# Performance work log

Hardware: AMD Instinct MI355X
Metric: run time of the kernel (lower is better)

The kernel has to match this reference:

```python
import jax, jax.numpy as jnp
import numpy as np

ALPHA = 0.1       # args.alpha
T = 1.0           # args.T temperature
SIGMA = 64.0      # Gaussian kernel bandwidth of kernel_function
B_CONST = 1.0     # B in get_lambda
N_ITERS = 50      # 2^-50 << tol=1e-8, matches the break condition of the 1000-iter loop
HW = 256          # image resolution (upsample target)


def _features(feat):
    # get_feature: bilinear upsample (align_corners=False == half-pixel, as jax.image.resize) then sigmoid(x/T)
    n, c, _, _ = feat.shape
    up = jax.image.resize(feat, (n, c, HW, HW), method='bilinear')
    return jax.nn.sigmoid(up / T)


def setup_inputs() -> dict:
    key = jax.random.key(0)
    k1, k2, k3, k4 = jax.random.split(key, 4)
    return {
        'cal_feat': jax.random.normal(k1, (256, 1, 64, 64), jnp.float32),
        'test_feat': jax.random.normal(k2, (32, 1, 64, 64), jnp.float32),
        'cal_gt': jax.random.randint(k3, (256, 1, 256, 256), 0, 2, jnp.int32),
        'test_gt': jax.random.randint(k4, (32, 1, 256, 256), 0, 2, jnp.int32),
    }


def reference(cal_feat, test_feat, cal_gt, test_gt):
    cal_res = _features(cal_feat)    # [N,1,H,W] in (0,1)
    test_res = _features(test_feat)  # [B,1,H,W]
    N = cal_res.shape[0]
    B = test_res.shape[0]
    f32 = cal_res.dtype

    # kernel_function.get_weight: Gaussian RBF on flattened features, plus self-weight 1, row-normalized -> [B, N+1]
    cf = cal_res.reshape(N, -1)
    tf = test_res.reshape(B, -1)
    d2 = (tf * tf).sum(-1)[:, None] + (cf * cf).sum(-1)[None, :] - 2.0 * (tf @ cf.T)
    k = jnp.exp(-d2 / (2.0 * SIGMA * SIGMA))
    w = jnp.concatenate([k, jnp.ones((B, 1), f32)], axis=1)
    w = w / w.sum(axis=1, keepdims=True)

    # FNR_i(t) = #{positive pixels of cal sample i with score < t} / #positives
    # (pred = res >= t, so false negatives are positive pixels with res < t). Precompute sorted
    # positive-pixel scores per cal sample so the bisection is a batched searchsorted.
    gt = (cal_gt > 0).reshape(N, -1)
    pos = jnp.sum(gt, axis=1)                                    # [N]
    scores = jnp.where(gt, cal_res.reshape(N, -1), jnp.inf)
    sorted_scores = jnp.sort(scores, axis=1)                     # [N, HW*HW], padding at +inf
    pos_f = jnp.maximum(pos, 1).astype(f32)

    def fnr_at(t):  # t: [B] thresholds -> [N, B]
        cnt = jax.vmap(lambda s: jnp.searchsorted(s, t, side='left'))(sorted_scores)
        return cnt.astype(f32) / pos_f[:, None]

    # batched bisection on lambda (get_lambda, vectorized over the B test samples)
    def body(carry, _):
        low, high = carry
        lam = 0.5 * (low + high)
        fnr = fnr_at(1.0 - lam)                                   # [N, B]
        risk = jnp.einsum('bn,nb->b', w[:, :-1], fnr) + w[:, -1] * B_CONST
        high = jnp.where(risk < ALPHA, lam, high)
        low = jnp.where(risk >= ALPHA, lam, low)
        return (low, high), None

    init = (jnp.zeros((B,), f32), jnp.ones((B,), f32))
    (low, _), _ = jax.lax.scan(body, init, None, length=N_ITERS)
    lam = low  # _lambda = low after the loop

    # prediction set, size and per-test FNR (get_fnr_list on the test sample)
    pred = test_res >= (1.0 - lam)[:, None, None, None]           # [B,1,H,W] bool
    size = jnp.sum(pred, axis=(1, 2, 3)).astype(f32)
    tgt = test_gt > 0
    tp = jnp.sum(pred & tgt, axis=(1, 2, 3)).astype(f32)
    tpos = jnp.maximum(jnp.sum(tgt, axis=(1, 2, 3)), 1).astype(f32)
    fnr_test = 1.0 - tp / tpos                                    # fdr_tensor, [B]
    return fnr_test, lam, size
```

## Files before the change

kernel.cpp:

```cpp
#include <hip/hip_runtime.h>


#define NPIX 65536
#define HB 16256
#define CDF_STRIDE 16272
#define ALPHA 0.1f

#define OFF_TESTRES  0
#define OFF_CALBF    8388608u
#define OFF_TESTBF   41943040u
#define OFF_GROUPED  46137344u
#define OFF_CDF      79691776u
#define OFF_GPART    96354304u
#define OFF_CC       98451456u
#define OFF_TT       98452480u
#define OFF_THR      98452608u
#define OFF_LAM      98452736u
#define OFF_FACC     98452864u

typedef __attribute__((ext_vector_type(8))) short bf16x8;
typedef __attribute__((ext_vector_type(16))) float f32x16;

__device__ __forceinline__ unsigned short f2bf_rne(float f) {
  unsigned u = __float_as_uint(f);
  return (unsigned short)((u + 0x7FFFu + ((u >> 16) & 1u)) >> 16);
}

__device__ __forceinline__ float score_at(const float* __restrict__ sfeat,
                                          int x0, int x1, float wx, int y) {
  float sy = 0.25f * (float)y - 0.375f;
  int y0 = (int)floorf(sy);
  float wy = sy - (float)y0;
  int y1 = y0 + 1;
  if (y0 < 0) y0 = 0;
  if (y1 > 63) y1 = 63;
  float a = sfeat[y0 * 64 + x0] * (1.f - wx) + sfeat[y0 * 64 + x1] * wx;
  float b = sfeat[y1 * 64 + x0] * (1.f - wx) + sfeat[y1 * 64 + x1] * wx;
  float v = a * (1.f - wy) + b * wy;
  return 1.f / (1.f + __expf(-v));
}

__global__ __launch_bounds__(1024, 8) void k_calt(const float* __restrict__ featc,
                                                  const int* __restrict__ gt,
                                                  unsigned short* __restrict__ calbf,
                                                  unsigned* __restrict__ cdf,
                                                  unsigned short* __restrict__ grouped,
                                                  float* __restrict__ cc,
                                                  const float* __restrict__ featt,
                                                  float* __restrict__ tres,
                                                  unsigned short* __restrict__ tbf,
                                                  float* __restrict__ tt) {
  __shared__ unsigned smem[16384];
  __shared__ float sfeat[4096];
  const int tid = threadIdx.x;
  const int lane = tid & 63, wv = tid >> 6;
  const int x = tid & 255, yq = tid >> 8;
  float sx = 0.25f * (float)x - 0.375f;
  int x0 = (int)floorf(sx);
  float wx = sx - (float)x0;
  int x1 = x0 + 1;
  if (x0 < 0) x0 = 0;
  if (x1 > 63) x1 = 63;

  if (blockIdx.x >= 256) {
    const int b = blockIdx.x - 256;
    for (int i = tid; i < 4096; i += 1024) sfeat[i] = featt[b * 4096 + i];
    __syncthreads();
    float* resb = tres + (size_t)b * NPIX;
    unsigned short* tbn = tbf + (size_t)b * NPIX;
    float sumsq = 0.f;
    #pragma unroll 4
    for (int it = 0; it < 64; ++it) {
      int y = it * 4 + yq;
      float s = score_at(sfeat, x0, x1, wx, y);
      int p = (y << 8) + x;
      resb[p] = s;
      unsigned short bh = f2bf_rne(s);
      tbn[p] = bh;
      float sr = __uint_as_float((unsigned)bh << 16);
      sumsq += sr * sr;
    }
    #pragma unroll
    for (int off = 32; off; off >>= 1) sumsq += __shfl_xor(sumsq, off);
    if (lane == 0) smem[wv] = __float_as_uint(sumsq);
    __syncthreads();
    if (tid == 0) {
      float t = 0.f;
      for (int w = 0; w < 16; ++w) t += __uint_as_float(smem[w]);
      tt[b] = t;
    }
    return;
  }

  const int n = blockIdx.x;
  for (int i = tid; i < HB; i += 1024) smem[i] = 0;
  for (int i = tid; i < 4096; i += 1024) sfeat[i] = featc[n * 4096 + i];
  const int* gtn = gt + (size_t)n * NPIX;
  unsigned short* cbn = calbf + (size_t)n * NPIX;
  __syncthreads();
  unsigned long long pm = 0ull;
  float sumsq = 0.f;
  #pragma unroll 4
  for (int it = 0; it < 64; ++it) {
    int y = it * 4 + yq;
    float s = score_at(sfeat, x0, x1, wx, y);
    int p = (y << 8) + x;
    unsigned short bh = f2bf_rne(s);
    cbn[p] = bh;
    float sr = __uint_as_float((unsigned)bh << 16);
    sumsq += sr * sr;
    if (gtn[p] > 0) {
      pm |= (1ull << it);
      atomicAdd(&smem[__float_as_uint(s) >> 16], 1u);
    }
  }
  #pragma unroll
  for (int off = 32; off; off >>= 1) sumsq += __shfl_xor(sumsq, off);
  if (lane == 0) smem[16336 + wv] = __float_as_uint(sumsq);
  __syncthreads();
  if (tid == 0) {
    float c = 0.f;
    for (int w = 0; w < 16; ++w) c += __uint_as_float(smem[16336 + w]);
    cc[n] = c;
  }
  unsigned* cdfn = cdf + (size_t)n * CDF_STRIDE;
  if (tid < 256) {
    const int base = tid * 64;
    unsigned psum = 0;
    if (base < HB) {
      for (int j = 0; j < 64; ++j) psum += smem[base + ((j + tid) & 63)];
    }
    unsigned inc = psum;
    #pragma unroll
    for (int off = 1; off < 64; off <<= 1) {
      unsigned v = __shfl_up(inc, off);
      if (lane >= off) inc += v;
    }
    if (lane == 63) smem[16320 + wv] = inc;
  }
  __syncthreads();
  if (tid < 256) {
    const int base = tid * 64;
    unsigned psum = 0;
    if (base < HB) {
      for (int j = 0; j < 64; ++j) psum += smem[base + ((j + tid) & 63)];
    }
    unsigned inc = psum;
    #pragma unroll
    for (int off = 1; off < 64; off <<= 1) {
      unsigned v = __shfl_up(inc, off);
      if (lane >= off) inc += v;
    }
    unsigned woff = 0;
    for (int w = 0; w < wv; ++w) woff += smem[16320 + w];
    unsigned run = woff + inc - psum;
    if (base < HB) {
      for (int j = 0; j < 64; ++j) {
        unsigned hcnt = smem[base + j];
        cdfn[base + j] = run;
        smem[base + j] = run;
        run += hcnt;
      }
    }
    if (tid == 255) cdfn[HB] = woff + inc;
  }
  __syncthreads();
  unsigned short* gn = grouped + (size_t)n * NPIX;
  for (int it = 0; it < 64; ++it) {
    if (pm & (1ull << it)) {
      int y = it * 4 + yq;
      float s = score_at(sfeat, x0, x1, wx, y);
      unsigned bits = __float_as_uint(s);
      unsigned idx = atomicAdd(&smem[bits >> 16], 1u);
      gn[idx] = (unsigned short)(bits & 0xFFFFu);
    }
  }
}

__global__ __launch_bounds__(256) void k_gemm(const unsigned short* __restrict__ tbf,
                                              const unsigned short* __restrict__ cbf,
                                              float* __restrict__ gpart) {
  __shared__ __align__(16) unsigned short As[16384];
  __shared__ __align__(16) unsigned short Bs[16384];
  __shared__ float lred[4][1024];
  const int tid = threadIdx.x;
  const int lane = tid & 63, wv = tid >> 6;
  const int r = lane & 31, half = lane >> 5;
  const int nt = blockIdx.x;
  f32x16 acc;
  #pragma unroll
  for (int i = 0; i < 16; ++i) acc[i] = 0.f;
  for (int ch = 0; ch < 2; ++ch) {
    const size_t kbase = (size_t)blockIdx.y * 1024 + ch * 512;
    __syncthreads();
    #pragma unroll
    for (int s = 0; s < 16; ++s) {
      int flat = s * 256 + tid;
      int rem = flat & 2047;
      int row = rem >> 6, kb = rem & 63;
      const unsigned short* src = (flat >= 2048)
          ? cbf + (size_t)(nt * 32 + row) * NPIX + kbase + kb * 8
          : tbf + (size_t)row * NPIX + kbase + kb * 8;
      int slot = ((kb << 5) + row) ^ (kb & 31);
      int4 v = *(const int4*)src;
      *(int4*)((flat >= 2048 ? Bs : As) + slot * 8) = v;
    }
    __syncthreads();
    #pragma unroll
    for (int i = 0; i < 8; ++i) {
      int k8 = (wv << 4) + i * 2 + half;
      int slot = ((k8 << 5) + r) ^ (k8 & 31);
      bf16x8 a = *(const bf16x8*)(As + slot * 8);
      bf16x8 b = *(const bf16x8*)(Bs + slot * 8);
      acc = __builtin_amdgcn_mfma_f32_32x32x16_bf16(a, b, acc, 0, 0, 0);
    }
  }
  #pragma unroll
  for (int rg = 0; rg < 16; ++rg) {
    int m = (rg & 3) + 8 * (rg >> 2) + 4 * half;
    lred[wv][m * 32 + r] = acc[rg];
  }
  __syncthreads();
  float* gp = gpart + (size_t)(blockIdx.y * 8 + nt) * 1024;
  for (int e = tid; e < 1024; e += 256)
    gp[e] = lred[0][e] + lred[1][e] + lred[2][e] + lred[3][e];
}

__global__ __launch_bounds__(512) void k_quant(const float* __restrict__ gpart,
                                               const float* __restrict__ cc,
                                               const float* __restrict__ tt,
                                               const unsigned* __restrict__ cdf,
                                               const unsigned short* __restrict__ grouped,
                                               float* __restrict__ lam,
                                               float* __restrict__ thr,
                                               int* __restrict__ facc) {
  __shared__ float qs[256];
  __shared__ float bins[4096];
  __shared__ float red[8];
  __shared__ float bc[2];
  __shared__ unsigned sBin;
  const int b = blockIdx.x, tid = threadIdx.x;
  const int lane = tid & 63, wv = tid >> 6;

  if (tid < 4) facc[b * 4 + tid] = 0;
  for (int i = tid; i < 4096; i += 512) bins[i] = 0.f;
  if (tid == 0) sBin = 0xFFFFFFFFu;

  float k = 0.f;
  if (tid < 256) {
    const float* gp = gpart + ((tid >> 5) * 1024) + (b * 32) + (tid & 31);
    float g = 0.f;
    #pragma unroll 8
    for (int ks = 0; ks < 64; ++ks) g += gp[(size_t)ks * 8192];
    float d2 = tt[b] + cc[tid] - 2.f * g;
    k = expf(-d2 * (1.f / 8192.f));
  }
  float v = k;
  #pragma unroll
  for (int off = 32; off; off >>= 1) v += __shfl_xor(v, off);
  if (lane == 0) red[wv] = v;
  __syncthreads();
  if (tid == 0) {
    float ws = 1.f;
    for (int w = 0; w < 8; ++w) ws += red[w];
    bc[0] = ws;
  }
  __syncthreads();
  const float wsum = bc[0];
  const float wlast = 1.f / wsum;
  const float R = ALPHA - wlast;
  if (R <= 0.f) {
    if (tid == 0) { lam[b] = 1.0f; thr[b] = 0.0f; }
    return;
  }
  if (tid < 256) {
    unsigned pos = cdf[(size_t)tid * CDF_STRIDE + HB];
    qs[tid] = k / (wsum * (float)(pos ? pos : 1u));
  }
  __syncthreads();

  int lo = 0, hi = HB;
  float baseS = 0.f;
  for (int it = 0; it < 14; ++it) {
    int mid = (lo + hi) >> 1;
    float p = 0.f;
    if (tid < 256) p = qs[tid] * (float)cdf[(size_t)tid * CDF_STRIDE + mid];
    float r = p;
    #pragma unroll
    for (int off = 32; off; off >>= 1) r += __shfl_xor(r, off);
    if (lane == 0) red[wv] = r;
    __syncthreads();
    if (tid == 0) {
      float s = 0.f;
      for (int w = 0; w < 8; ++w) s += red[w];
      bc[1] = s;
    }
    __syncthreads();
    float S = bc[1];
    if (S < R) { lo = mid; baseS = S; } else { hi = mid; }
  }
  const int B = lo;

  {
    const int n = tid >> 1;
    const float q = qs[n];
    const unsigned* cn = cdf + (size_t)n * CDF_STRIDE;
    const unsigned short* gn = grouped + (size_t)n * NPIX;
    unsigned e0 = cn[B + 1];
    for (unsigned j = cn[B] + (tid & 1); j < e0; j += 2)
      atomicAdd(&bins[gn[j] >> 4], q);
  }
  __syncthreads();

  if (wv == 0) {
    float s = 0.f;
    for (int j = 0; j < 64; ++j) s += bins[lane * 64 + j];
    float inc = s;
    #pragma unroll
    for (int off = 1; off < 64; off <<= 1) {
      float u = __shfl_up(inc, off);
      if (lane >= off) inc += u;
    }
    float pre = inc - s;
    bool hit = (baseS + pre < R) && (baseS + inc >= R);
    unsigned long long m = __ballot(hit);
    int ow = m ? (__ffsll((unsigned long long)m) - 1) : -1;
    if (lane == ow) {
      float run = baseS + pre;
      unsigned bin = (unsigned)lane * 64 + 63;
      for (int j = 0; j < 64; ++j) {
        float bv = bins[lane * 64 + j];
        if (run + bv >= R) { bin = (unsigned)lane * 64 + j; break; }
        run += bv;
      }
      sBin = bin;
    }
    if (m == 0 && lane == 0) sBin = 4095u;
  }
  __syncthreads();
  if (tid == 0) {
    unsigned tb = ((unsigned)B << 16) | (sBin << 4);
    lam[b] = 1.0f - __uint_as_float(tb | 0x8u);
    thr[b] = __uint_as_float((tb | 0xFu) + 1u);
  }
}

__global__ __launch_bounds__(256) void k_finalp(const float* __restrict__ tres,
                                                const int* __restrict__ tgt,
                                                const float* __restrict__ thr,
                                                int* __restrict__ facc) {
  __shared__ int red[12];
  const int b = blockIdx.x, seg = blockIdx.y, tid = threadIdx.x;
  const int lane = tid & 63, wv = tid >> 6;
  const float th = thr[b];
  const float* rb = tres + (size_t)b * NPIX + seg * 8192;
  const int* gb = tgt + (size_t)b * NPIX + seg * 8192;
  int sz = 0, tp = 0, tpos = 0;
  for (int i = 0; i < 32; ++i) {
    int p = i * 256 + tid;
    int pred = (rb[p] >= th) ? 1 : 0;
    int tg = (gb[p] > 0) ? 1 : 0;
    sz += pred;
    tp += pred & tg;
    tpos += tg;
  }
  #pragma unroll
  for (int off = 32; off; off >>= 1) {
    sz += __shfl_xor(sz, off);
    tp += __shfl_xor(tp, off);
    tpos += __shfl_xor(tpos, off);
  }
  if (lane == 0) { red[wv] = sz; red[4 + wv] = tp; red[8 + wv] = tpos; }
  __syncthreads();
  if (tid == 0) {
    int s0 = red[0] + red[1] + red[2] + red[3];
    int s1 = red[4] + red[5] + red[6] + red[7];
    int s2 = red[8] + red[9] + red[10] + red[11];
    atomicAdd(&facc[b * 4 + 0], s0);
    atomicAdd(&facc[b * 4 + 1], s1);
    atomicAdd(&facc[b * 4 + 2], s2);
  }
}

__global__ void k_out(const int* __restrict__ facc, const float* __restrict__ lam,
                      float* __restrict__ out) {
  int b = threadIdx.x;
  if (b < 32) {
    int sz = facc[b * 4], tp = facc[b * 4 + 1], tpos = facc[b * 4 + 2];
    float tposf = (float)(tpos > 0 ? tpos : 1);
    out[b] = 1.f - (float)tp / tposf;
    out[32 + b] = lam[b];
    out[64 + b] = (float)sz;
  }
}

extern "C" void kernel_launch(void* const* d_in, const int* in_sizes, int n_in,
                              void* d_out, int out_size, void* d_ws, size_t ws_size,
                              hipStream_t stream) {
  const float* cal_feat = (const float*)d_in[0];
  const float* test_feat = (const float*)d_in[1];
  const int* cal_gt = (const int*)d_in[2];
  const int* test_gt = (const int*)d_in[3];
  float* out = (float*)d_out;
  char* ws = (char*)d_ws;

  float* test_res = (float*)(ws + OFF_TESTRES);
  unsigned short* cal_bf = (unsigned short*)(ws + OFF_CALBF);
  unsigned short* test_bf = (unsigned short*)(ws + OFF_TESTBF);
  unsigned short* grouped = (unsigned short*)(ws + OFF_GROUPED);
  unsigned* cdf = (unsigned*)(ws + OFF_CDF);
  float* gpart = (float*)(ws + OFF_GPART);
  float* cc = (float*)(ws + OFF_CC);
  float* tt = (float*)(ws + OFF_TT);
  float* thr = (float*)(ws + OFF_THR);
  float* lam = (float*)(ws + OFF_LAM);
  int* facc = (int*)(ws + OFF_FACC);

  k_calt<<<dim3(288), dim3(1024), 0, stream>>>(cal_feat, cal_gt, cal_bf, cdf, grouped, cc,
                                               test_feat, test_res, test_bf, tt);
  k_gemm<<<dim3(8, 64), dim3(256), 0, stream>>>(test_bf, cal_bf, gpart);
  k_quant<<<dim3(32), dim3(512), 0, stream>>>(gpart, cc, tt, cdf, grouped, lam, thr, facc);
  k_finalp<<<dim3(32, 8), dim3(256), 0, stream>>>(test_res, test_gt, thr, facc);
  k_out<<<dim3(1), dim3(64), 0, stream>>>(facc, lam, out);
}
```

Before: 245.7 us.

## Fold test feature upsampling into calibration blocks and move test norms to quant kernel

Removes the 32 separate test-sample blocks from the first kernel. Each of the 256 calibration blocks now upsamples 32 rows of one test image after its own work, reading the test features directly from global memory. The test squared-norm reduction moves into k_quant, which re-reads the bf16 test image. The CDF is now written to global in one coalesced pass from shared memory instead of inside the serial per-thread scan loop. Unroll and occupancy hints are also changed. The aim is to balance the tail of the first kernel and to cut strided global writes, at the cost of extra work serialized in k_quant.

```diff
diff --git a/kernel.cpp b/kernel.cpp
--- a/kernel.cpp
+++ b/kernel.cpp
@@ -13,10 +13,9 @@
 #define OFF_CDF      79691776u
 #define OFF_GPART    96354304u
 #define OFF_CC       98451456u
-#define OFF_TT       98452480u
-#define OFF_THR      98452608u
-#define OFF_LAM      98452736u
-#define OFF_FACC     98452864u
+#define OFF_THR      98452480u
+#define OFF_LAM      98452608u
+#define OFF_FACC     98452736u
 
 typedef __attribute__((ext_vector_type(8))) short bf16x8;
 typedef __attribute__((ext_vector_type(16))) float f32x16;
@@ -26,7 +25,7 @@
   return (unsigned short)((u + 0x7FFFu + ((u >> 16) & 1u)) >> 16);
 }
 
-__device__ __forceinline__ float score_at(const float* __restrict__ sfeat,
+__device__ __forceinline__ float score_at(const float* __restrict__ src,
                                           int x0, int x1, float wx, int y) {
   float sy = 0.25f * (float)y - 0.375f;
   int y0 = (int)floorf(sy);
@@ -34,73 +33,40 @@
   int y1 = y0 + 1;
   if (y0 < 0) y0 = 0;
   if (y1 > 63) y1 = 63;
-  float a = sfeat[y0 * 64 + x0] * (1.f - wx) + sfeat[y0 * 64 + x1] * wx;
-  float b = sfeat[y1 * 64 + x0] * (1.f - wx) + sfeat[y1 * 64 + x1] * wx;
+  float a = src[y0 * 64 + x0] * (1.f - wx) + src[y0 * 64 + x1] * wx;
+  float b = src[y1 * 64 + x0] * (1.f - wx) + src[y1 * 64 + x1] * wx;
   float v = a * (1.f - wy) + b * wy;
   return 1.f / (1.f + __expf(-v));
 }
 
-__global__ __launch_bounds__(1024, 8) void k_calt(const float* __restrict__ featc,
-                                                  const int* __restrict__ gt,
-                                                  unsigned short* __restrict__ calbf,
-                                                  unsigned* __restrict__ cdf,
-                                                  unsigned short* __restrict__ grouped,
-                                                  float* __restrict__ cc,
-                                                  const float* __restrict__ featt,
-                                                  float* __restrict__ tres,
-                                                  unsigned short* __restrict__ tbf,
-                                                  float* __restrict__ tt) {
+__global__ __launch_bounds__(1024, 4) void k_cal(const float* __restrict__ featc,
+                                                 const int* __restrict__ gt,
+                                                 unsigned short* __restrict__ calbf,
+                                                 unsigned* __restrict__ cdf,
+                                                 unsigned short* __restrict__ grouped,
+                                                 float* __restrict__ cc,
+                                                 const float* __restrict__ featt,
+                                                 float* __restrict__ tres,
+                                                 unsigned short* __restrict__ tbf) {
   __shared__ unsigned smem[16384];
   __shared__ float sfeat[4096];
-  const int tid = threadIdx.x;
+  const int n = blockIdx.x, tid = threadIdx.x;
   const int lane = tid & 63, wv = tid >> 6;
   const int x = tid & 255, yq = tid >> 8;
+  for (int i = tid; i < 16320; i += 1024) smem[i] = 0;
+  for (int i = tid; i < 4096; i += 1024) sfeat[i] = featc[n * 4096 + i];
+  const int* gtn = gt + (size_t)n * NPIX;
+  unsigned short* cbn = calbf + (size_t)n * NPIX;
   float sx = 0.25f * (float)x - 0.375f;
   int x0 = (int)floorf(sx);
   float wx = sx - (float)x0;
   int x1 = x0 + 1;
   if (x0 < 0) x0 = 0;
   if (x1 > 63) x1 = 63;
-
-  if (blockIdx.x >= 256) {
-    const int b = blockIdx.x - 256;
-    for (int i = tid; i < 4096; i += 1024) sfeat[i] = featt[b * 4096 + i];
-    __syncthreads();
-    float* resb = tres + (size_t)b * NPIX;
-    unsigned short* tbn = tbf + (size_t)b * NPIX;
-    float sumsq = 0.f;
-    #pragma unroll 4
-    for (int it = 0; it < 64; ++it) {
-      int y = it * 4 + yq;
-      float s = score_at(sfeat, x0, x1, wx, y);
-      int p = (y << 8) + x;
-      resb[p] = s;
-      unsigned short bh = f2bf_rne(s);
-      tbn[p] = bh;
-      float sr = __uint_as_float((unsigned)bh << 16);
-      sumsq += sr * sr;
-    }
-    #pragma unroll
-    for (int off = 32; off; off >>= 1) sumsq += __shfl_xor(sumsq, off);
-    if (lane == 0) smem[wv] = __float_as_uint(sumsq);
-    __syncthreads();
-    if (tid == 0) {
-      float t = 0.f;
-      for (int w = 0; w < 16; ++w) t += __uint_as_float(smem[w]);
-      tt[b] = t;
-    }
-    return;
-  }
-
-  const int n = blockIdx.x;
-  for (int i = tid; i < HB; i += 1024) smem[i] = 0;
-  for (int i = tid; i < 4096; i += 1024) sfeat[i] = featc[n * 4096 + i];
-  const int* gtn = gt + (size_t)n * NPIX;
-  unsigned short* cbn = calbf + (size_t)n * NPIX;
   __syncthreads();
   unsigned long long pm = 0ull;
   float sumsq = 0.f;
-  #pragma unroll 4
+  #pragma unroll 8
   for (int it = 0; it < 64; ++it) {
     int y = it * 4 + yq;
     float s = score_at(sfeat, x0, x1, wx, y);
@@ -156,14 +122,15 @@
     unsigned run = woff + inc - psum;
     if (base < HB) {
       for (int j = 0; j < 64; ++j) {
-        unsigned hcnt = smem[base + j];
-        cdfn[base + j] = run;
+        unsigned h = smem[base + j];
         smem[base + j] = run;
-        run += hcnt;
+        run += h;
       }
     }
     if (tid == 255) cdfn[HB] = woff + inc;
   }
+  __syncthreads();
+  for (int i = tid; i < HB; i += 1024) cdfn[i] = smem[i];
   __syncthreads();
   unsigned short* gn = grouped + (size_t)n * NPIX;
   for (int it = 0; it < 64; ++it) {
@@ -174,6 +141,18 @@
       unsigned idx = atomicAdd(&smem[bits >> 16], 1u);
       gn[idx] = (unsigned short)(bits & 0xFFFFu);
     }
+  }
+  const int tb2 = n >> 3, ybase = (n & 7) * 32;
+  const float* tfp = featt + tb2 * 4096;
+  float* resb = tres + (size_t)tb2 * NPIX;
+  unsigned short* tbn = tbf + (size_t)tb2 * NPIX;
+  #pragma unroll
+  for (int i = 0; i < 8; ++i) {
+    int y = ybase + (i << 2) + yq;
+    float s = score_at(tfp, x0, x1, wx, y);
+    int p = (y << 8) + x;
+    resb[p] = s;
+    tbn[p] = f2bf_rne(s);
   }
 }
 
@@ -228,16 +207,16 @@
 
 __global__ __launch_bounds__(512) void k_quant(const float* __restrict__ gpart,
                                                const float* __restrict__ cc,
-                                               const float* __restrict__ tt,
                                                const unsigned* __restrict__ cdf,
                                                const unsigned short* __restrict__ grouped,
+                                               const unsigned short* __restrict__ tbf,
                                                float* __restrict__ lam,
                                                float* __restrict__ thr,
                                                int* __restrict__ facc) {
   __shared__ float qs[256];
   __shared__ float bins[4096];
   __shared__ float red[8];
-  __shared__ float bc[2];
+  __shared__ float bc[4];
   __shared__ unsigned sBin;
   const int b = blockIdx.x, tid = threadIdx.x;
   const int lane = tid & 63, wv = tid >> 6;
@@ -245,6 +224,33 @@
   if (tid < 4) facc[b * 4 + tid] = 0;
   for (int i = tid; i < 4096; i += 512) bins[i] = 0.f;
   if (tid == 0) sBin = 0xFFFFFFFFu;
+
+  float ts = 0.f;
+  const int4* tbp = (const int4*)(tbf + (size_t)b * NPIX);
+  for (int i = tid; i < 8192; i += 512) {
+    int4 v = tbp[i];
+    unsigned w0 = (unsigned)v.x, w1 = (unsigned)v.y, w2 = (unsigned)v.z, w3 = (unsigned)v.w;
+    float f;
+    f = __uint_as_float(w0 << 16); ts += f * f;
+    f = __uint_as_float(w0 & 0xFFFF0000u); ts += f * f;
+    f = __uint_as_float(w1 << 16); ts += f * f;
+    f = __uint_as_float(w1 & 0xFFFF0000u); ts += f * f;
+    f = __uint_as_float(w2 << 16); ts += f * f;
+    f = __uint_as_float(w2 & 0xFFFF0000u); ts += f * f;
+    f = __uint_as_float(w3 << 16); ts += f * f;
+    f = __uint_as_float(w3 & 0xFFFF0000u); ts += f * f;
+  }
+  #pragma unroll
+  for (int off = 32; off; off >>= 1) ts += __shfl_xor(ts, off);
+  if (lane == 0) red[wv] = ts;
+  __syncthreads();
+  if (tid == 0) {
+    float t = 0.f;
+    for (int w = 0; w < 8; ++w) t += red[w];
+    bc[0] = t;
+  }
+  __syncthreads();
+  const float ttv = bc[0];
 
   float k = 0.f;
   if (tid < 256) {
@@ -252,7 +258,7 @@
     float g = 0.f;
     #pragma unroll 8
     for (int ks = 0; ks < 64; ++ks) g += gp[(size_t)ks * 8192];
-    float d2 = tt[b] + cc[tid] - 2.f * g;
+    float d2 = ttv + cc[tid] - 2.f * g;
     k = expf(-d2 * (1.f / 8192.f));
   }
   float v = k;
@@ -263,10 +269,10 @@
   if (tid == 0) {
     float ws = 1.f;
     for (int w = 0; w < 8; ++w) ws += red[w];
-    bc[0] = ws;
-  }
-  __syncthreads();
-  const float wsum = bc[0];
+    bc[1] = ws;
+  }
+  __syncthreads();
+  const float wsum = bc[1];
   const float wlast = 1.f / wsum;
   const float R = ALPHA - wlast;
   if (R <= 0.f) {
@@ -293,10 +299,10 @@
     if (tid == 0) {
       float s = 0.f;
       for (int w = 0; w < 8; ++w) s += red[w];
-      bc[1] = s;
+      bc[2] = s;
     }
     __syncthreads();
-    float S = bc[1];
+    float S = bc[2];
     if (S < R) { lo = mid; baseS = S; } else { hi = mid; }
   }
   const int B = lo;
@@ -411,15 +417,14 @@
   unsigned* cdf = (unsigned*)(ws + OFF_CDF);
   float* gpart = (float*)(ws + OFF_GPART);
   float* cc = (float*)(ws + OFF_CC);
-  float* tt = (float*)(ws + OFF_TT);
   float* thr = (float*)(ws + OFF_THR);
   float* lam = (float*)(ws + OFF_LAM);
   int* facc = (int*)(ws + OFF_FACC);
 
-  k_calt<<<dim3(288), dim3(1024), 0, stream>>>(cal_feat, cal_gt, cal_bf, cdf, grouped, cc,
-                                               test_feat, test_res, test_bf, tt);
+  k_cal<<<dim3(256), dim3(1024), 0, stream>>>(cal_feat, cal_gt, cal_bf, cdf, grouped, cc,
+                                              test_feat, test_res, test_bf);
   k_gemm<<<dim3(8, 64), dim3(256), 0, stream>>>(test_bf, cal_bf, gpart);
-  k_quant<<<dim3(32), dim3(512), 0, stream>>>(gpart, cc, tt, cdf, grouped, lam, thr, facc);
+  k_quant<<<dim3(32), dim3(512), 0, stream>>>(gpart, cc, cdf, grouped, test_bf, lam, thr, facc);
   k_finalp<<<dim3(32, 8), dim3(256), 0, stream>>>(test_res, test_gt, thr, facc);
   k_out<<<dim3(1), dim3(64), 0, stream>>>(facc, lam, out);
 }
```

After: 249.4 us. About the same (+1.5%).
